# Kernel tuning notes

Measured on AMD Instinct MI355X. Metric: run time of the kernel, lower is better.

Reference implementation:

```python
import jax, jax.numpy as jnp
import numpy as np

COMMITMENT_COST = 0.25


def setup_inputs() -> dict:
    key = jax.random.key(0)
    k1, k2 = jax.random.split(key)
    inputs = jax.random.normal(k1, (32, 512, 32, 32), dtype=jnp.float32)
    embeddings = jax.random.normal(k2, (4096, 512), dtype=jnp.float32)
    return {"inputs": inputs, "embeddings": embeddings}


def reference(inputs, embeddings):
    # NCHW -> NHWC, flatten to (N, D)
    x = jnp.transpose(inputs, (0, 2, 3, 1))  # [B,H,W,D]
    D = embeddings.shape[1]
    z = x.reshape(-1, D)  # [N,D]

    # Squared L2 distances: ||z||^2 - 2 z E^T + ||E||^2
    d1 = jnp.sum(z * z, axis=1, keepdims=True)            # [N,1]
    d2 = 2.0 * jnp.matmul(z, embeddings.T)                # [N,K]
    d3 = jnp.sum(embeddings * embeddings, axis=1)[None]   # [1,K]
    distances = d1 - d2 + d3                              # [N,K]

    k = jnp.argmin(distances, axis=1)                     # [N]
    q = embeddings[k]                                     # [N,D] gather

    # latent loss: codebook loss + commitment loss
    e_loss = jnp.mean((jax.lax.stop_gradient(z) - q) ** 2)
    q_loss = COMMITMENT_COST * jnp.mean((z - jax.lax.stop_gradient(q)) ** 2)
    loss = e_loss + q_loss

    qx = q.reshape(x.shape)                               # [B,H,W,D]
    output = jnp.transpose(qx, (0, 3, 1, 2))              # NCHW
    return output, loss
```

## Files before the change

kernel.cpp:

```cpp
#include <hip/hip_runtime.h>

#define N_PTS 32768
#define DIM   512
#define KCODES 4096
#define HW    1024
#define MARGIN 0.125f
#define MAXFLAG 2048

typedef _Float16 half8 __attribute__((ext_vector_type(8)));
typedef float f32x4 __attribute__((ext_vector_type(4)));
typedef unsigned long long u64;

#define E16_OFF   0
#define BIAS_OFF  4194304
#define TOP2_OFF  4210688
#define ZC_OFF    5259264


__device__ __forceinline__ unsigned mono(float f) {
    unsigned u = __float_as_uint(f);
    return (u & 0x80000000u) ? ~u : (u | 0x80000000u);
}
__device__ __forceinline__ float unmono(unsigned m) {
    unsigned u = (m & 0x80000000u) ? (m & 0x7FFFFFFFu) : ~m;
    return __uint_as_float(u);
}

#define ASYNC16(src, dst) __builtin_amdgcn_global_load_lds( \
    (const __attribute__((address_space(1))) void*)(src), \
    (__attribute__((address_space(3))) void*)(dst), 16, 0, 0)

__global__ void prep_e_kernel(const float* __restrict__ E, _Float16* __restrict__ E16,
                              float* __restrict__ bias) {
    int k = blockIdx.x;
    int l = threadIdx.x;
    const float4* row = (const float4*)(E + (size_t)k * DIM);
    float4 a = row[l * 2];
    float4 b = row[l * 2 + 1];
    half8 h;
    h[0] = (_Float16)a.x; h[1] = (_Float16)a.y; h[2] = (_Float16)a.z; h[3] = (_Float16)a.w;
    h[4] = (_Float16)b.x; h[5] = (_Float16)b.y; h[6] = (_Float16)b.z; h[7] = (_Float16)b.w;
    *(half8*)(E16 + (size_t)k * DIM + l * 8) = h;
    float s = a.x * a.x + a.y * a.y + a.z * a.z + a.w * a.w +
              b.x * b.x + b.y * b.y + b.z * b.z + b.w * b.w;
#pragma unroll
    for (int off = 32; off > 0; off >>= 1) s += __shfl_down(s, off, 64);
    if (l == 0) bias[k] = 0.5f * s;
}

__global__ __launch_bounds__(256, 2) void score16_kernel(
    const float* __restrict__ in, const _Float16* __restrict__ E16,
    const float* __restrict__ bias, u64* __restrict__ top2)
{
    __shared__ alignas(16) _Float16 stage[2][2048 * 8];

    const int t    = threadIdx.x;
    const int lane = t & 63;
    const int w    = t >> 6;
    const int lm   = lane & 15;
    const int lq   = lane >> 4;
    const int ks   = blockIdx.x;
    const int pt0  = blockIdx.y * 128;

    half8 zf[2][16];
#pragma unroll
    for (int pt = 0; pt < 2; pt++) {
        const int n = pt0 + 32 * w + 16 * pt + lm;
        const float* zb = in + (size_t)(n >> 10) * (DIM * HW) + (n & 1023);
#pragma unroll
        for (int kc = 0; kc < 16; kc++) {
            const int d0 = kc * 32 + lq * 8;
            half8 h;
#pragma unroll
            for (int j = 0; j < 8; j++) h[j] = (_Float16)zb[(size_t)(d0 + j) << 10];
            zf[pt][kc] = h;
        }
    }

    const u64 PKNEG = ((u64)0x007FFFFFu) << 32;
    u64 b1[2], b2[2];
    float thr2[2];
#pragma unroll
    for (int p = 0; p < 2; p++) { b1[p] = PKNEG; b2[p] = PKNEG; thr2[p] = -INFINITY; }

    {
        const int code0 = ks * 2048;
#pragma unroll
        for (int i = 0; i < 8; i++) {
            const int kc = 4 * w + (i >> 1);
            const int ct = i & 1;
            ASYNC16(E16 + (size_t)(code0 + ct * 16 + lm) * DIM + kc * 32 + lq * 8,
                    &stage[0][(size_t)(w * 512 + i * 64) << 3]);
        }
    }

    for (int f = 0; f < 64; f++) {
        const int code0 = ks * 2048 + f * 32;
        const int buf = f & 1;
        __syncthreads();
        {
            const int cn = ks * 2048 + ((f + 1) & 63) * 32;
#pragma unroll
            for (int i = 0; i < 8; i++) {
                const int kc = 4 * w + (i >> 1);
                const int ct = i & 1;
                ASYNC16(E16 + (size_t)(cn + ct * 16 + lm) * DIM + kc * 32 + lq * 8,
                        &stage[buf ^ 1][(size_t)(w * 512 + i * 64) << 3]);
            }
        }
        f32x4 acc[2][2];
#pragma unroll
        for (int ct = 0; ct < 2; ct++) {
            const float4 bv = *(const float4*)&bias[code0 + ct * 16 + lq * 4];
            f32x4 bi; bi[0] = -bv.x; bi[1] = -bv.y; bi[2] = -bv.z; bi[3] = -bv.w;
            acc[ct][0] = bi; acc[ct][1] = bi;
        }
#pragma unroll
        for (int kc = 0; kc < 16; kc++) {
            half8 a0 = *(const half8*)&stage[buf][(size_t)(kc * 128 + lane) << 3];
            half8 a1 = *(const half8*)&stage[buf][(size_t)(kc * 128 + 64 + lane) << 3];
            acc[0][0] = __builtin_amdgcn_mfma_f32_16x16x32_f16(a0, zf[0][kc], acc[0][0], 0, 0, 0);
            acc[0][1] = __builtin_amdgcn_mfma_f32_16x16x32_f16(a0, zf[1][kc], acc[0][1], 0, 0, 0);
            acc[1][0] = __builtin_amdgcn_mfma_f32_16x16x32_f16(a1, zf[0][kc], acc[1][0], 0, 0, 0);
            acc[1][1] = __builtin_amdgcn_mfma_f32_16x16x32_f16(a1, zf[1][kc], acc[1][1], 0, 0, 0);
        }
#pragma unroll
        for (int pt = 0; pt < 2; pt++) {
#pragma unroll
            for (int ct = 0; ct < 2; ct++) {
                f32x4 a = acc[ct][pt];
                bool hit = (a[0] > thr2[pt]) | (a[1] > thr2[pt]) |
                           (a[2] > thr2[pt]) | (a[3] > thr2[pt]);
                if (__any(hit)) {
#pragma unroll
                    for (int r = 0; r < 4; r++) {
                        float v = a[r];
                        if (v > thr2[pt]) {
                            int code = code0 + ct * 16 + lq * 4 + r;
                            u64 pk = ((u64)mono(v) << 32) | (unsigned)(0xFFFu ^ (unsigned)code);
                            if (pk > b1[pt]) { b2[pt] = b1[pt]; b1[pt] = pk; }
                            else if (pk > b2[pt]) { b2[pt] = pk; }
                            thr2[pt] = unmono((unsigned)(b2[pt] >> 32));
                        }
                    }
                }
            }
        }
    }
#pragma unroll
    for (int pt = 0; pt < 2; pt++) {
#pragma unroll
        for (int m = 16; m <= 32; m <<= 1) {
            u64 o1 = __shfl_xor(b1[pt], m, 64);
            u64 o2 = __shfl_xor(b2[pt], m, 64);
            u64 m1 = b1[pt] > o1 ? b1[pt] : o1;
            u64 lo = b1[pt] > o1 ? o1 : b1[pt];
            u64 mm = b2[pt] > o2 ? b2[pt] : o2;
            b2[pt] = lo > mm ? lo : mm;
            b1[pt] = m1;
        }
    }
    if (lq == 0) {
#pragma unroll
        for (int pt = 0; pt < 2; pt++) {
            const size_t p = (size_t)(pt0 + 32 * w + 16 * pt + lm);
            top2[p * 4 + ks * 2]     = b1[pt];
            top2[p * 4 + ks * 2 + 1] = b2[pt];
        }
    }
}

__global__ void merge_compact_kernel(const u64* __restrict__ top2, const float* __restrict__ in,
                                     int* __restrict__ k_final, int* __restrict__ list,
                                     int* __restrict__ count, float* __restrict__ zc) {
    int pt = blockIdx.x * 256 + threadIdx.x;
    const u64* p = top2 + (size_t)pt * 4;
    u64 B1 = 0, B2 = 0;
#pragma unroll
    for (int ks = 0; ks < 2; ks++) {
        u64 p1 = p[ks * 2], p2 = p[ks * 2 + 1];
        u64 m1 = B1 > p1 ? B1 : p1;
        u64 lo = B1 > p1 ? p1 : B1;
        u64 mm = B2 > p2 ? B2 : p2;
        B2 = lo > mm ? lo : mm;
        B1 = m1;
    }
    k_final[pt] = 0xFFF ^ (int)(B1 & 0xFFFull);
    float s1 = unmono((unsigned)(B1 >> 32));
    float s2 = unmono((unsigned)(B2 >> 32));
    if (s1 - s2 < MARGIN) {
        int idx = atomicAdd(count, 1);
        if (idx < MAXFLAG) {
            list[idx] = pt;
            const float* zb = in + (size_t)(pt >> 10) * (DIM * HW) + (pt & 1023);
            float* dst = zc + (size_t)idx * DIM;
#pragma unroll 8
            for (int d = 0; d < DIM; d++) dst[d] = zb[(size_t)d << 10];
        }
    }
}

__global__ __launch_bounds__(256) void rescore_kernel(
    const float* __restrict__ zc, const float* __restrict__ E,
    const float* __restrict__ bias, const int* __restrict__ count,
    u64* __restrict__ rb)
{
    __shared__ float As[16][128];
    __shared__ float Bs[16][132];

    int cnt = *count; if (cnt > MAXFLAG) cnt = MAXFLAG;
    const int t  = threadIdx.x;
    const int k0 = blockIdx.x * 128;
    const int r0 = blockIdx.y * 128;
    if (r0 >= cnt) return;

    float acc[8][8];
#pragma unroll
    for (int i = 0; i < 8; i++)
#pragma unroll
        for (int j = 0; j < 8; j++) acc[i][j] = 0.f;

    const int ra = (t >> 4) << 2;
    const int cb = (t & 15) << 2;

    for (int d0 = 0; d0 < DIM; d0 += 16) {
        {
            int j   = t >> 2;
            int dd4 = (t & 3) << 2;
            int rA = r0 + j;        if (rA >= cnt) rA = cnt - 1;
            int rB = r0 + j + 64;   if (rB >= cnt) rB = cnt - 1;
            float4 v0 = *(const float4*)&zc[(size_t)rA * DIM + d0 + dd4];
            float4 v1 = *(const float4*)&zc[(size_t)rB * DIM + d0 + dd4];
            As[dd4 + 0][j] = v0.x; As[dd4 + 1][j] = v0.y;
            As[dd4 + 2][j] = v0.z; As[dd4 + 3][j] = v0.w;
            As[dd4 + 0][j + 64] = v1.x; As[dd4 + 1][j + 64] = v1.y;
            As[dd4 + 2][j + 64] = v1.z; As[dd4 + 3][j + 64] = v1.w;
        }
        {
            int j   = t >> 2;
            int dd4 = (t & 3) << 2;
            const float* p = E + (size_t)(k0 + j) * DIM + d0 + dd4;
            float4 v0 = *(const float4*)p;
            float4 v1 = *(const float4*)(p + (size_t)64 * DIM);
            Bs[dd4 + 0][j] = v0.x; Bs[dd4 + 1][j] = v0.y;
            Bs[dd4 + 2][j] = v0.z; Bs[dd4 + 3][j] = v0.w;
            Bs[dd4 + 0][j + 64] = v1.x; Bs[dd4 + 1][j + 64] = v1.y;
            Bs[dd4 + 2][j + 64] = v1.z; Bs[dd4 + 3][j + 64] = v1.w;
        }
        __syncthreads();
#pragma unroll
        for (int dd = 0; dd < 16; dd++) {
            float4 a0 = *(const float4*)&As[dd][ra];
            float4 a1 = *(const float4*)&As[dd][ra + 64];
            float4 b0 = *(const float4*)&Bs[dd][cb];
            float4 b1v = *(const float4*)&Bs[dd][cb + 64];
            float av[8] = {a0.x, a0.y, a0.z, a0.w, a1.x, a1.y, a1.z, a1.w};
            float bv[8] = {b0.x, b0.y, b0.z, b0.w, b1v.x, b1v.y, b1v.z, b1v.w};
#pragma unroll
            for (int i = 0; i < 8; i++)
#pragma unroll
                for (int j = 0; j < 8; j++)
                    acc[i][j] = fmaf(av[i], bv[j], acc[i][j]);
        }
        __syncthreads();
    }

    float bcol[8];
#pragma unroll
    for (int j = 0; j < 8; j++) {
        int k = k0 + ((j < 4) ? (cb + j) : (64 + cb + j - 4));
        bcol[j] = bias[k];
    }
    u64 pk[8];
#pragma unroll
    for (int i = 0; i < 8; i++) {
        u64 bestp = 0ull;
#pragma unroll
        for (int j = 0; j < 8; j++) {
            int k = k0 + ((j < 4) ? (cb + j) : (64 + cb + j - 4));
            float s = acc[i][j] - bcol[j];
            u64 p = ((u64)mono(s) << 32) | (u64)(~(unsigned)k);
            if (p > bestp) bestp = p;
        }
        pk[i] = bestp;
    }
#pragma unroll
    for (int i = 0; i < 8; i++) {
#pragma unroll
        for (int off = 8; off > 0; off >>= 1) {
            u64 o = __shfl_down(pk[i], off, 16);
            if (o > pk[i]) pk[i] = o;
        }
    }
    if ((t & 15) == 0) {
#pragma unroll
        for (int i = 0; i < 8; i++) {
            int row = r0 + ((i < 4) ? (ra + i) : (64 + ra + i - 4));
            int slot = row < cnt ? row : cnt - 1;
            atomicMax(&rb[slot], pk[i]);
        }
    }
}

__global__ void apply_kernel(const int* __restrict__ list, const int* __restrict__ count,
                             const u64* __restrict__ rb, int* __restrict__ k_final) {
    int i = blockIdx.x * 256 + threadIdx.x;
    int cnt = *count; if (cnt > MAXFLAG) cnt = MAXFLAG;
    if (i < cnt) k_final[list[i]] = (int)(~(unsigned)(rb[i] & 0xffffffffull));
}

__global__ void gather_kernel(const float* __restrict__ in, const float* __restrict__ E,
                              const int* __restrict__ k_final,
                              float* __restrict__ out, float* __restrict__ sumsq)
{
    const int t  = threadIdx.x;
    const int tx = t & 63;
    const int ty = t >> 6;
    const int n  = blockIdx.x * 64 + tx;
    const int k  = k_final[n];
    const float* erow = E + (size_t)k * DIM;
    const size_t base = (size_t)(n >> 10) * (DIM * HW) + (n & 1023);
    float local = 0.f;
    for (int d = ty; d < DIM; d += 4) {
        float q = erow[d];
        size_t idx = base + ((size_t)d << 10);
        float z = in[idx];
        out[idx] = q;
        float df = z - q;
        local = fmaf(df, df, local);
    }
#pragma unroll
    for (int off = 32; off > 0; off >>= 1) local += __shfl_down(local, off, 64);
    __shared__ float red[4];
    if (tx == 0) red[ty] = local;
    __syncthreads();
    if (t == 0) atomicAdd(sumsq, red[0] + red[1] + red[2] + red[3]);
}

__global__ void finalize_kernel(const float* __restrict__ sumsq, float* __restrict__ out_loss) {
    *out_loss = 1.25f * (*sumsq) * (1.0f / 16777216.0f);
}

extern "C" void kernel_launch(void* const* d_in, const int* in_sizes, int n_in,
                              void* d_out, int out_size, void* d_ws, size_t ws_size,
                              hipStream_t stream) {
    const float* in = (const float*)d_in[0];
    const float* E  = (const float*)d_in[1];
    float* out = (float*)d_out;
    char* ob = (char*)d_out;

    _Float16* E16 = (_Float16*)(ob + E16_OFF);
    float* bias   = (float*)(ob + BIAS_OFF);
    u64* top2     = (u64*)(ob + TOP2_OFF);
    float* zc     = (float*)(ob + ZC_OFF);

    u64* rb      = (u64*)d_ws;
    int* count   = (int*)((char*)d_ws + 16384);
    float* sumsq = (float*)((char*)d_ws + 16388);
    int* list    = (int*)((char*)d_ws + 16392);
    int* k_final = (int*)((char*)d_ws + 24584);

    hipMemsetAsync(d_ws, 0, 16392, stream);

    prep_e_kernel<<<KCODES, 64, 0, stream>>>(E, E16, bias);

    score16_kernel<<<dim3(2, 256), 256, 0, stream>>>(in, E16, bias, top2);

    merge_compact_kernel<<<128, 256, 0, stream>>>(top2, in, k_final, list, count, zc);

    rescore_kernel<<<dim3(32, 16), 256, 0, stream>>>(zc, E, bias, count, rb);
    apply_kernel<<<8, 256, 0, stream>>>(list, count, rb, k_final);

    gather_kernel<<<N_PTS / 64, 256, 0, stream>>>(in, E, k_final, out, sumsq);
    finalize_kernel<<<1, 1, 0, stream>>>(sumsq, out + 16777216);
}
```

Baseline: 503.8 us.

## Split codebook staging into half-tiles with four-buffer async pipeline and shared bias

Replaces the double-buffered full 32-code tile staging with four half-tile LDS buffers (each covering half the embedding dimension), prefetching two half-tiles ahead and using manual vmcnt waits plus raw s_barrier instead of __syncthreads. The bias slice for the block is also loaded once into shared memory asynchronously rather than read from global each iteration. The intent is to keep more loads in flight and hide global-load latency behind MFMA work, at the cost of more barriers per iteration and reliance on hand-counted vmcnt values being correct.

Measured after the change: 515.4 us. 2.3% more time.

```diff
diff --git a/kernel.cpp b/kernel.cpp
--- a/kernel.cpp
+++ b/kernel.cpp
@@ -52,7 +52,8 @@
     const float* __restrict__ in, const _Float16* __restrict__ E16,
     const float* __restrict__ bias, u64* __restrict__ top2)
 {
-    __shared__ alignas(16) _Float16 stage[2][2048 * 8];
+    __shared__ alignas(16) _Float16 stage[4][1024 * 8];
+    __shared__ alignas(16) float bias_sm[2048];
 
     const int t    = threadIdx.x;
     const int lane = t & 63;
@@ -76,6 +77,27 @@
             zf[pt][kc] = h;
         }
     }
+    asm volatile("s_waitcnt vmcnt(0)" ::: "memory");
+
+#pragma unroll
+    for (int i = 0; i < 2; i++)
+        ASYNC16(bias + ks * 2048 + (w * 2 + i) * 256 + lane * 4,
+                &bias_sm[(w * 2 + i) * 256]);
+
+    auto stage_half = [&](int b, int fn, int hn) {
+        const int cn = ks * 2048 + (fn & 63) * 32;
+#pragma unroll
+        for (int i = 0; i < 4; i++) {
+            const int kcp = 2 * w + (i >> 1);
+            const int ct  = i & 1;
+            ASYNC16(E16 + (size_t)(cn + ct * 16 + lm) * DIM + hn * 256 + kcp * 32 + lq * 8,
+                    &stage[b][(size_t)(256 * w + 64 * i) << 3]);
+        }
+    };
+
+    stage_half(0, 0, 0);
+    stage_half(1, 0, 1);
+    stage_half(2, 1, 0);
 
     const u64 PKNEG = ((u64)0x007FFFFFu) << 32;
     u64 b1[2], b2[2];
@@ -83,46 +105,46 @@
 #pragma unroll
     for (int p = 0; p < 2; p++) { b1[p] = PKNEG; b2[p] = PKNEG; thr2[p] = -INFINITY; }
 
-    {
-        const int code0 = ks * 2048;
-#pragma unroll
-        for (int i = 0; i < 8; i++) {
-            const int kc = 4 * w + (i >> 1);
-            const int ct = i & 1;
-            ASYNC16(E16 + (size_t)(code0 + ct * 16 + lm) * DIM + kc * 32 + lq * 8,
-                    &stage[0][(size_t)(w * 512 + i * 64) << 3]);
-        }
-    }
-
     for (int f = 0; f < 64; f++) {
         const int code0 = ks * 2048 + f * 32;
-        const int buf = f & 1;
-        __syncthreads();
-        {
-            const int cn = ks * 2048 + ((f + 1) & 63) * 32;
-#pragma unroll
-            for (int i = 0; i < 8; i++) {
-                const int kc = 4 * w + (i >> 1);
-                const int ct = i & 1;
-                ASYNC16(E16 + (size_t)(cn + ct * 16 + lm) * DIM + kc * 32 + lq * 8,
-                        &stage[buf ^ 1][(size_t)(w * 512 + i * 64) << 3]);
-            }
-        }
+        const int bA = (2 * f) & 3;
+        const int bB = (2 * f + 1) & 3;
+
         f32x4 acc[2][2];
+
+        asm volatile("s_waitcnt vmcnt(8)" ::: "memory");
+        __builtin_amdgcn_s_barrier();
+        asm volatile("" ::: "memory");
+        stage_half((2 * f + 3) & 3, f + 1, 1);
 #pragma unroll
         for (int ct = 0; ct < 2; ct++) {
-            const float4 bv = *(const float4*)&bias[code0 + ct * 16 + lq * 4];
+            const float4 bv = *(const float4*)&bias_sm[f * 32 + ct * 16 + lq * 4];
             f32x4 bi; bi[0] = -bv.x; bi[1] = -bv.y; bi[2] = -bv.z; bi[3] = -bv.w;
             acc[ct][0] = bi; acc[ct][1] = bi;
         }
 #pragma unroll
-        for (int kc = 0; kc < 16; kc++) {
-            half8 a0 = *(const half8*)&stage[buf][(size_t)(kc * 128 + lane) << 3];
-            half8 a1 = *(const half8*)&stage[buf][(size_t)(kc * 128 + 64 + lane) << 3];
+        for (int kc = 0; kc < 8; kc++) {
+            half8 a0 = *(const half8*)&stage[bA][(size_t)(kc * 128 + lane) << 3];
+            half8 a1 = *(const half8*)&stage[bA][(size_t)(kc * 128 + 64 + lane) << 3];
             acc[0][0] = __builtin_amdgcn_mfma_f32_16x16x32_f16(a0, zf[0][kc], acc[0][0], 0, 0, 0);
             acc[0][1] = __builtin_amdgcn_mfma_f32_16x16x32_f16(a0, zf[1][kc], acc[0][1], 0, 0, 0);
             acc[1][0] = __builtin_amdgcn_mfma_f32_16x16x32_f16(a1, zf[0][kc], acc[1][0], 0, 0, 0);
             acc[1][1] = __builtin_amdgcn_mfma_f32_16x16x32_f16(a1, zf[1][kc], acc[1][1], 0, 0, 0);
+        }
+        asm volatile("s_waitcnt lgkmcnt(0)" ::: "memory");
+
+        asm volatile("s_waitcnt vmcnt(8)" ::: "memory");
+        __builtin_amdgcn_s_barrier();
+        asm volatile("" ::: "memory");
+        stage_half((2 * f + 4) & 3, f + 2, 0);
+#pragma unroll
+        for (int kc = 0; kc < 8; kc++) {
+            half8 a0 = *(const half8*)&stage[bB][(size_t)(kc * 128 + lane) << 3];
+            half8 a1 = *(const half8*)&stage[bB][(size_t)(kc * 128 + 64 + lane) << 3];
+            acc[0][0] = __builtin_amdgcn_mfma_f32_16x16x32_f16(a0, zf[0][8 + kc], acc[0][0], 0, 0, 0);
+            acc[0][1] = __builtin_amdgcn_mfma_f32_16x16x32_f16(a0, zf[1][8 + kc], acc[0][1], 0, 0, 0);
+            acc[1][0] = __builtin_amdgcn_mfma_f32_16x16x32_f16(a1, zf[0][8 + kc], acc[1][0], 0, 0, 0);
+            acc[1][1] = __builtin_amdgcn_mfma_f32_16x16x32_f16(a1, zf[1][8 + kc], acc[1][1], 0, 0, 0);
         }
 #pragma unroll
         for (int pt = 0; pt < 2; pt++) {
@@ -146,7 +168,10 @@
                 }
             }
         }
-    }
+        asm volatile("s_waitcnt lgkmcnt(0)" ::: "memory");
+    }
+    asm volatile("s_waitcnt vmcnt(0)" ::: "memory");
+
 #pragma unroll
     for (int pt = 0; pt < 2; pt++) {
 #pragma unroll
```

## Fold apply step into gather and parallelize flagged-row copy across wavefronts

Applied to the files above, without the earlier changes.

Removes the apply kernel by encoding the flagged-slot index into the high bits of k_final, so the gather kernel resolves the rescored code directly from rb. In merge_compact, flagged points are first collected in shared memory, then each wavefront copies a whole 512-float row with 64 lanes instead of one thread serially copying it. This saves a kernel launch and replaces a serial per-thread strided copy with lane-parallel loads. The cost is extra shared-memory atomics and barriers plus one dependent rb load in gather for flagged points.

Result: faster. 490.8 us (-2.6%).

```diff
diff --git a/kernel.cpp b/kernel.cpp
--- a/kernel.cpp
+++ b/kernel.cpp
@@ -171,9 +171,14 @@
 }
 
 __global__ void merge_compact_kernel(const u64* __restrict__ top2, const float* __restrict__ in,
-                                     int* __restrict__ k_final, int* __restrict__ list,
+                                     int* __restrict__ k_final,
                                      int* __restrict__ count, float* __restrict__ zc) {
-    int pt = blockIdx.x * 256 + threadIdx.x;
+    __shared__ unsigned loc[256];
+    __shared__ int nloc;
+    const int t = threadIdx.x;
+    if (t == 0) nloc = 0;
+    __syncthreads();
+    const int pt = blockIdx.x * 256 + t;
     const u64* p = top2 + (size_t)pt * 4;
     u64 B1 = 0, B2 = 0;
 #pragma unroll
@@ -185,17 +190,32 @@
         B2 = lo > mm ? lo : mm;
         B1 = m1;
     }
-    k_final[pt] = 0xFFF ^ (int)(B1 & 0xFFFull);
+    const int code = 0xFFF ^ (int)(B1 & 0xFFFull);
     float s1 = unmono((unsigned)(B1 >> 32));
     float s2 = unmono((unsigned)(B2 >> 32));
+    int fi = -1;
     if (s1 - s2 < MARGIN) {
         int idx = atomicAdd(count, 1);
         if (idx < MAXFLAG) {
-            list[idx] = pt;
-            const float* zb = in + (size_t)(pt >> 10) * (DIM * HW) + (pt & 1023);
-            float* dst = zc + (size_t)idx * DIM;
-#pragma unroll 8
-            for (int d = 0; d < DIM; d++) dst[d] = zb[(size_t)d << 10];
+            fi = idx;
+            int l = atomicAdd(&nloc, 1);
+            loc[l] = ((unsigned)t << 16) | (unsigned)idx;
+        }
+    }
+    k_final[pt] = code | ((fi + 1) << 12);
+    __syncthreads();
+    const int n = nloc;
+    const int wv = t >> 6, lane = t & 63;
+    for (int i = wv; i < n; i += 4) {
+        const unsigned e = loc[i];
+        const int lpt = blockIdx.x * 256 + (int)(e >> 16);
+        const int idx = (int)(e & 0xFFFFu);
+        const float* zb = in + (size_t)(lpt >> 10) * (DIM * HW) + (lpt & 1023);
+        float* dst = zc + (size_t)idx * DIM;
+#pragma unroll
+        for (int j = 0; j < 8; j++) {
+            const int d = j * 64 + lane;
+            dst[d] = zb[(size_t)d << 10];
         }
     }
 }
@@ -302,22 +322,18 @@
     }
 }
 
-__global__ void apply_kernel(const int* __restrict__ list, const int* __restrict__ count,
-                             const u64* __restrict__ rb, int* __restrict__ k_final) {
-    int i = blockIdx.x * 256 + threadIdx.x;
-    int cnt = *count; if (cnt > MAXFLAG) cnt = MAXFLAG;
-    if (i < cnt) k_final[list[i]] = (int)(~(unsigned)(rb[i] & 0xffffffffull));
-}
-
 __global__ void gather_kernel(const float* __restrict__ in, const float* __restrict__ E,
-                              const int* __restrict__ k_final,
+                              const int* __restrict__ k_final, const u64* __restrict__ rb,
                               float* __restrict__ out, float* __restrict__ sumsq)
 {
     const int t  = threadIdx.x;
     const int tx = t & 63;
     const int ty = t >> 6;
     const int n  = blockIdx.x * 64 + tx;
-    const int k  = k_final[n];
+    const int v  = k_final[n];
+    int k = v & 0xFFF;
+    const int fi = (v >> 12) - 1;
+    if (fi >= 0) k = (int)(~(unsigned)(rb[fi] & 0xffffffffull));
     const float* erow = E + (size_t)k * DIM;
     const size_t base = (size_t)(n >> 10) * (DIM * HW) + (n & 1023);
     float local = 0.f;
@@ -357,7 +373,6 @@
     u64* rb      = (u64*)d_ws;
     int* count   = (int*)((char*)d_ws + 16384);
     float* sumsq = (float*)((char*)d_ws + 16388);
-    int* list    = (int*)((char*)d_ws + 16392);
     int* k_final = (int*)((char*)d_ws + 24584);
 
     hipMemsetAsync(d_ws, 0, 16392, stream);
@@ -366,11 +381,10 @@
 
     score16_kernel<<<dim3(2, 256), 256, 0, stream>>>(in, E16, bias, top2);
 
-    merge_compact_kernel<<<128, 256, 0, stream>>>(top2, in, k_final, list, count, zc);
+    merge_compact_kernel<<<128, 256, 0, stream>>>(top2, in, k_final, count, zc);
 
     rescore_kernel<<<dim3(32, 16), 256, 0, stream>>>(zc, E, bias, count, rb);
-    apply_kernel<<<8, 256, 0, stream>>>(list, count, rb, k_final);
-
-    gather_kernel<<<N_PTS / 64, 256, 0, stream>>>(in, E, k_final, out, sumsq);
+
+    gather_kernel<<<N_PTS / 64, 256, 0, stream>>>(in, E, k_final, rb, out, sumsq);
     finalize_kernel<<<1, 1, 0, stream>>>(sumsq, out + 16777216);
 }
```
